# Performance work log

Hardware: AMD Instinct MI355X
Metric: run time of the kernel (lower is better)

The kernel has to match this reference:

```python
import jax, jax.numpy as jnp
import numpy as np

NUM_USERS = 100000
NUM_ITEMS = 50000
N_NODES = NUM_USERS + NUM_ITEMS
EMBED_DIM = 64
N_EDGES = 2400000
NUM_LAYERS = 3
DROPOUT_P = 0.2


def setup_inputs() -> dict:
    key = jax.random.key(0)
    k1, k2, k3, k4, k5 = jax.random.split(key, 5)
    # xavier_uniform bound = sqrt(6/(fan_in+fan_out))
    bu = np.sqrt(6.0 / (NUM_USERS + EMBED_DIM)).astype(np.float32)
    bi = np.sqrt(6.0 / (NUM_ITEMS + EMBED_DIM)).astype(np.float32)
    user_emb = jax.random.uniform(k1, (NUM_USERS, EMBED_DIM), jnp.float32, -bu, bu)
    item_emb = jax.random.uniform(k2, (NUM_ITEMS, EMBED_DIM), jnp.float32, -bi, bi)
    adj_rows = jax.random.randint(k3, (N_EDGES,), 0, N_NODES, dtype=jnp.int32)
    adj_cols = jax.random.randint(k4, (N_EDGES,), 0, N_NODES, dtype=jnp.int32)
    # normalized adjacency values (positive, small) mimicking D^-1/2 A D^-1/2
    adj_vals = jax.random.uniform(k5, (N_EDGES,), jnp.float32, 0.0, 0.25)
    return {"user_emb": user_emb, "item_emb": item_emb,
            "adj_rows": adj_rows, "adj_cols": adj_cols, "adj_vals": adj_vals}


def _spmm(rows, cols, vals, x):
    # y[r] += vals[e] * x[cols[e]] for each edge e with rows[e]==r
    gathered = x[cols] * vals[:, None]          # [E, D]
    return jax.ops.segment_sum(gathered, rows, num_segments=N_NODES)


def reference(user_emb, item_emb, adj_rows, adj_cols, adj_vals):
    x = jnp.concatenate([user_emb, item_emb], axis=0)          # [N, D]
    # dropout (training=True), fixed key for determinism
    keep = jax.random.bernoulli(jax.random.key(42), 1.0 - DROPOUT_P, x.shape)
    x = jnp.where(keep, x / (1.0 - DROPOUT_P), 0.0)
    acc = x  # running sum over layer embeddings (== mean * (L+1))
    for _ in range(NUM_LAYERS):
        x = _spmm(adj_rows, adj_cols, adj_vals, x)
        acc = acc + x
    final = acc / jnp.float32(NUM_LAYERS + 1)
    return final[:NUM_USERS], final[NUM_USERS:]
```

## Files before the change

kernel.cpp:

```cpp
#include <hip/hip_runtime.h>


static constexpr int NU = 100000;
static constexpr int NI = 50000;
static constexpr int NN = NU + NI;
static constexpr int D  = 64;
static constexpr int E  = 2400000;
static constexpr int XN = NN * D;
static constexpr int XH = XN / 2;
static constexpr int NB = (NN + 1023) >> 10;
static constexpr int BPC = 24000;
static constexpr int BIN_T = 256;
static constexpr int BIN_U = 16;
static constexpr int BIN_CHUNK = BIN_T * BIN_U;

typedef _Float16 half_t;
typedef _Float16 half8 __attribute__((ext_vector_type(8)));

__device__ __forceinline__ unsigned rotl32(unsigned x, int r) {
    return (x << r) | (x >> (32 - r));
}

__device__ __forceinline__ void threefry2x32(unsigned k0, unsigned k1,
                                             unsigned x0, unsigned x1,
                                             unsigned& o0, unsigned& o1) {
    unsigned ks2 = k0 ^ k1 ^ 0x1BD11BDAu;
    x0 += k0; x1 += k1;
#define TF_R(r) { x0 += x1; x1 = rotl32(x1, r); x1 ^= x0; }
    TF_R(13) TF_R(15) TF_R(26) TF_R(6)   x0 += k1;  x1 += ks2 + 1u;
    TF_R(17) TF_R(29) TF_R(16) TF_R(24)  x0 += ks2; x1 += k0 + 2u;
    TF_R(13) TF_R(15) TF_R(26) TF_R(6)   x0 += k0;  x1 += k1 + 3u;
    TF_R(17) TF_R(29) TF_R(16) TF_R(24)  x0 += k1;  x1 += ks2 + 4u;
    TF_R(13) TF_R(15) TF_R(26) TF_R(6)   x0 += ks2; x1 += k0 + 5u;
#undef TF_R
    o0 = x0; o1 = x1;
}

__device__ __forceinline__ float dropout_val(const float* __restrict__ ue,
                                             const float* __restrict__ ie,
                                             int i, unsigned bits) {
    float src = (i < NU * D) ? ue[i] : ie[i - NU * D];
    float u = __uint_as_float((bits >> 9) | 0x3f800000u) - 1.0f;
    return (u < 0.8f) ? (src / 0.8f) : 0.0f;
}

__global__ void k_dropout_init(const float* __restrict__ ue,
                               const float* __restrict__ ie,
                               half_t* __restrict__ x0h) {
    int j = blockIdx.x * blockDim.x + threadIdx.x;
    if (j >= XH) return;
    unsigned o0, o1, b0, b1;
    threefry2x32(0u, 42u, 0u, (unsigned)j, o0, o1);        b0 = o0 ^ o1;
    threefry2x32(0u, 42u, 0u, (unsigned)(j + XH), o0, o1); b1 = o0 ^ o1;
    x0h[j]      = (half_t)dropout_val(ue, ie, j, b0);
    x0h[j + XH] = (half_t)dropout_val(ue, ie, j + XH, b1);
}

__global__ void __launch_bounds__(BIN_T) k_bin(const int* __restrict__ rows,
                                               const int* __restrict__ cols,
                                               const float* __restrict__ vals,
                                               int2* __restrict__ stg,
                                               int* __restrict__ pcnt) {
    __shared__ int lcnt[NB];
    __shared__ int gbase[NB];
    int tid = threadIdx.x;
    for (int i = tid; i < NB; i += BIN_T) lcnt[i] = 0;
    __syncthreads();
    int base = blockIdx.x * BIN_CHUNK;
    int lp[BIN_U];
    int2 rec[BIN_U];
    #pragma unroll
    for (int u = 0; u < BIN_U; ++u) {
        int idx = base + u * BIN_T + tid;
        if (idx < E) {
            int row = rows[idx];
            int col = cols[idx];
            float v = vals[idx];
            unsigned q = min(__float2int_rn(v * 65536.f), 16383);
            int b = row >> 10;
            int loff = atomicAdd(&lcnt[b], 1);
            lp[u] = (b << 13) | loff;
            rec[u] = make_int2((int)((q << 18) | (unsigned)col), row);
        } else {
            lp[u] = -1;
        }
    }
    __syncthreads();
    for (int i = tid; i < NB; i += BIN_T)
        gbase[i] = atomicAdd(&pcnt[i * 16], lcnt[i]);
    __syncthreads();
    #pragma unroll
    for (int u = 0; u < BIN_U; ++u) {
        if (lp[u] >= 0) {
            int b = lp[u] >> 13;
            int pos = gbase[b] + (lp[u] & 8191);
            if (pos < BPC) stg[(size_t)b * BPC + pos] = rec[u];
        }
    }
}

__global__ void k_bscan(const int* __restrict__ pcnt, int* __restrict__ bbase,
                        int* __restrict__ rp) {
    int lane = threadIdx.x;
    int carry = 0;
    for (int base = 0; base < NB; base += 64) {
        int i = base + lane;
        int v = (i < NB) ? pcnt[i * 16] : 0;
        int x = v;
        #pragma unroll
        for (int d = 1; d < 64; d <<= 1) {
            int y = __shfl_up(x, d);
            if (lane >= d) x += y;
        }
        if (i < NB) bbase[i] = carry + x - v;
        carry += __shfl(x, 63);
    }
    if (lane == 0) rp[NN] = E;
}

__global__ void __launch_bounds__(1024) k_bsort(const int2* __restrict__ stg,
                                                const int* __restrict__ pcnt,
                                                const int* __restrict__ bbase,
                                                int* __restrict__ rp,
                                                unsigned* __restrict__ ev) {
    __shared__ int cnt[1024];
    __shared__ int wsum[16];
    int b = blockIdx.x;
    int t = threadIdx.x;
    cnt[t] = 0;
    __syncthreads();
    int tot = min(pcnt[b * 16], BPC);
    int bb = bbase[b];
    const int2* s = stg + (size_t)b * BPC;
    for (int i = t; i < tot; i += 1024)
        atomicAdd(&cnt[s[i].y & 1023], 1);
    __syncthreads();
    int v = cnt[t];
    int lane = t & 63, w = t >> 6;
    int x = v;
    #pragma unroll
    for (int d = 1; d < 64; d <<= 1) {
        int y = __shfl_up(x, d);
        if (lane >= d) x += y;
    }
    if (lane == 63) wsum[w] = x;
    __syncthreads();
    if (w == 0 && lane < 16) {
        int sv = wsum[lane];
        #pragma unroll
        for (int d = 1; d < 16; d <<= 1) {
            int y = __shfl_up(sv, d);
            if (lane >= d) sv += y;
        }
        wsum[lane] = sv;
    }
    __syncthreads();
    int excl = ((w > 0) ? wsum[w - 1] : 0) + x - v;
    int row = (b << 10) + t;
    if (row < NN) rp[row] = bb + excl;
    __syncthreads();
    cnt[t] = bb + excl;
    __syncthreads();
    for (int i = t; i < tot; i += 1024) {
        int2 r = s[i];
        int pos = atomicAdd(&cnt[r.y & 1023], 1);
        ev[pos] = (unsigned)r.x;
    }
}

template <int MODE>
__global__ void __launch_bounds__(256) k_spmm(const int* __restrict__ rp,
                                              const unsigned* __restrict__ ev,
                                              const half_t* __restrict__ xh,
                                              half_t* __restrict__ yh,
                                              const half_t* __restrict__ x0h,
                                              const half_t* __restrict__ y1h,
                                              float* __restrict__ out) {
    int wid  = threadIdx.x >> 6;
    int lane = threadIdx.x & 63;
    int g    = lane >> 3;
    int l    = lane & 7;
    int row  = blockIdx.x * 32 + wid * 8 + g;
    if (row >= NN) return;
    const float inv = 1.0f / 65536.0f;
    int s0  = rp[row];
    int cnt = rp[row + 1] - s0;
    float acc[8] = {0.f, 0.f, 0.f, 0.f, 0.f, 0.f, 0.f, 0.f};
    int gl = g << 3;
    for (int base = 0; base < cnt; base += 8) {
        int idx = base + l;
        int pc = (idx < cnt) ? (int)ev[s0 + idx] : 0;
        #pragma unroll
        for (int j = 0; j < 8; j += 2) {
            int p0 = __shfl(pc, gl | j);
            int p1 = __shfl(pc, gl | (j + 1));
            int   c0 = p0 & 0x3FFFF;
            float v0 = (float)((unsigned)p0 >> 18) * inv;
            int   c1 = p1 & 0x3FFFF;
            float v1 = (float)((unsigned)p1 >> 18) * inv;
            const half8 xa = *(const half8*)(xh + c0 * 64 + l * 8);
            const half8 xb = *(const half8*)(xh + c1 * 64 + l * 8);
            #pragma unroll
            for (int k = 0; k < 8; ++k) acc[k] = fmaf(v0, (float)xa[k], acc[k]);
            #pragma unroll
            for (int k = 0; k < 8; ++k) acc[k] = fmaf(v1, (float)xb[k], acc[k]);
        }
    }
    int o = row * 64 + l * 8;
    if (MODE == 0) {
        half8 st;
        #pragma unroll
        for (int k = 0; k < 8; ++k) st[k] = (half_t)acc[k];
        *(half8*)(yh + o) = st;
    } else {
        const half8 a0 = *(const half8*)(x0h + o);
        const half8 a1 = *(const half8*)(y1h + o);
        const half8 a2 = *(const half8*)(xh + o);
        float r[8];
        #pragma unroll
        for (int k = 0; k < 8; ++k)
            r[k] = ((float)a0[k] + (float)a1[k] + (float)a2[k] + acc[k]) * 0.25f;
        *(float4*)(out + o)     = make_float4(r[0], r[1], r[2], r[3]);
        *(float4*)(out + o + 4) = make_float4(r[4], r[5], r[6], r[7]);
    }
}

extern "C" void kernel_launch(void* const* d_in, const int* in_sizes, int n_in,
                              void* d_out, int out_size, void* d_ws, size_t ws_size,
                              hipStream_t stream) {
    const float* ue   = (const float*)d_in[0];
    const float* ie   = (const float*)d_in[1];
    const int*   rows = (const int*)d_in[2];
    const int*   cols = (const int*)d_in[3];
    const float* vals = (const float*)d_in[4];
    float* out = (float*)d_out;

    half_t*   X0h   = (half_t*)d_ws;
    half_t*   Y1h   = X0h + XN;
    half_t*   Y2h   = Y1h + XN;
    int2*     stg   = (int2*)Y1h;
    unsigned* ev    = (unsigned*)(Y2h + XN);
    int*      rp    = (int*)(ev + E);
    int*      pcnt  = rp + NN + 4;
    int*      bbase = pcnt + NB * 16;

    (void)hipMemsetAsync(pcnt, 0, (NB * 16 + NB) * sizeof(int), stream);
    k_dropout_init<<<(XH + 255) / 256, 256, 0, stream>>>(ue, ie, X0h);
    k_bin<<<(E + BIN_CHUNK - 1) / BIN_CHUNK, BIN_T, 0, stream>>>(rows, cols, vals, stg, pcnt);
    k_bscan<<<1, 64, 0, stream>>>(pcnt, bbase, rp);
    k_bsort<<<NB, 1024, 0, stream>>>(stg, pcnt, bbase, rp, ev);

    int sgrid = (NN + 31) / 32;
    k_spmm<0><<<sgrid, 256, 0, stream>>>(rp, ev, X0h, Y1h, nullptr, nullptr, nullptr);
    k_spmm<0><<<sgrid, 256, 0, stream>>>(rp, ev, Y1h, Y2h, nullptr, nullptr, nullptr);
    k_spmm<1><<<sgrid, 256, 0, stream>>>(rp, ev, Y2h, nullptr, X0h, Y1h, out);
}
```

Baseline: 318.6 us.

## Merge dropout into binning kernel, fold bucket scan into sort, batch SpMM gathers

Fuses the dropout-init kernel into the binning kernel as extra blocks and removes the single-block bucket scan by having each sort block compute its own prefix over bucket counts. This cuts two kernel launches and their serialization gaps. The SpMM inner loop now prefetches the next edge chunk and issues all eight row gathers before accumulating, to expose more memory-level parallelism. The cost is more registers in SpMM and a redundant O(NB) prefix sum per sort block.

```diff
diff --git a/kernel.cpp b/kernel.cpp
--- a/kernel.cpp
+++ b/kernel.cpp
@@ -13,6 +13,8 @@
 static constexpr int BIN_T = 256;
 static constexpr int BIN_U = 16;
 static constexpr int BIN_CHUNK = BIN_T * BIN_U;
+static constexpr int BGRID = (E + BIN_CHUNK - 1) / BIN_CHUNK;
+static constexpr int DGRID = (XH + 255) / 256;
 
 typedef _Float16 half_t;
 typedef _Float16 half8 __attribute__((ext_vector_type(8)));
@@ -44,26 +46,27 @@
     return (u < 0.8f) ? (src / 0.8f) : 0.0f;
 }
 
-__global__ void k_dropout_init(const float* __restrict__ ue,
-                               const float* __restrict__ ie,
-                               half_t* __restrict__ x0h) {
-    int j = blockIdx.x * blockDim.x + threadIdx.x;
-    if (j >= XH) return;
-    unsigned o0, o1, b0, b1;
-    threefry2x32(0u, 42u, 0u, (unsigned)j, o0, o1);        b0 = o0 ^ o1;
-    threefry2x32(0u, 42u, 0u, (unsigned)(j + XH), o0, o1); b1 = o0 ^ o1;
-    x0h[j]      = (half_t)dropout_val(ue, ie, j, b0);
-    x0h[j + XH] = (half_t)dropout_val(ue, ie, j + XH, b1);
-}
-
-__global__ void __launch_bounds__(BIN_T) k_bin(const int* __restrict__ rows,
+__global__ void __launch_bounds__(BIN_T) k_pre(const int* __restrict__ rows,
                                                const int* __restrict__ cols,
                                                const float* __restrict__ vals,
                                                int2* __restrict__ stg,
-                                               int* __restrict__ pcnt) {
+                                               int* __restrict__ pcnt,
+                                               const float* __restrict__ ue,
+                                               const float* __restrict__ ie,
+                                               half_t* __restrict__ x0h) {
     __shared__ int lcnt[NB];
     __shared__ int gbase[NB];
     int tid = threadIdx.x;
+    if (blockIdx.x >= BGRID) {
+        int j = (blockIdx.x - BGRID) * BIN_T + tid;
+        if (j >= XH) return;
+        unsigned o0, o1, b0, b1;
+        threefry2x32(0u, 42u, 0u, (unsigned)j, o0, o1);        b0 = o0 ^ o1;
+        threefry2x32(0u, 42u, 0u, (unsigned)(j + XH), o0, o1); b1 = o0 ^ o1;
+        x0h[j]      = (half_t)dropout_val(ue, ie, j, b0);
+        x0h[j + XH] = (half_t)dropout_val(ue, ie, j + XH, b1);
+        return;
+    }
     for (int i = tid; i < NB; i += BIN_T) lcnt[i] = 0;
     __syncthreads();
     int base = blockIdx.x * BIN_CHUNK;
@@ -99,38 +102,27 @@
     }
 }
 
-__global__ void k_bscan(const int* __restrict__ pcnt, int* __restrict__ bbase,
-                        int* __restrict__ rp) {
-    int lane = threadIdx.x;
-    int carry = 0;
-    for (int base = 0; base < NB; base += 64) {
-        int i = base + lane;
-        int v = (i < NB) ? pcnt[i * 16] : 0;
-        int x = v;
-        #pragma unroll
-        for (int d = 1; d < 64; d <<= 1) {
-            int y = __shfl_up(x, d);
-            if (lane >= d) x += y;
-        }
-        if (i < NB) bbase[i] = carry + x - v;
-        carry += __shfl(x, 63);
-    }
-    if (lane == 0) rp[NN] = E;
-}
-
 __global__ void __launch_bounds__(1024) k_bsort(const int2* __restrict__ stg,
                                                 const int* __restrict__ pcnt,
-                                                const int* __restrict__ bbase,
                                                 int* __restrict__ rp,
                                                 unsigned* __restrict__ ev) {
     __shared__ int cnt[1024];
     __shared__ int wsum[16];
+    __shared__ int sbb;
     int b = blockIdx.x;
     int t = threadIdx.x;
     cnt[t] = 0;
+    if (t < 64) {
+        int a = 0;
+        for (int i = t; i < b; i += 64) a += pcnt[i * 16];
+        #pragma unroll
+        for (int d = 1; d < 64; d <<= 1) a += __shfl_xor(a, d);
+        if (t == 0) sbb = a;
+    }
+    if (b == 0 && t == 0) rp[NN] = E;
     __syncthreads();
     int tot = min(pcnt[b * 16], BPC);
-    int bb = bbase[b];
+    int bb = sbb;
     const int2* s = stg + (size_t)b * BPC;
     for (int i = t; i < tot; i += 1024)
         atomicAdd(&cnt[s[i].y & 1023], 1);
@@ -187,24 +179,25 @@
     int cnt = rp[row + 1] - s0;
     float acc[8] = {0.f, 0.f, 0.f, 0.f, 0.f, 0.f, 0.f, 0.f};
     int gl = g << 3;
+    int pc = (l < cnt) ? (int)ev[s0 + l] : 0;
     for (int base = 0; base < cnt; base += 8) {
-        int idx = base + l;
-        int pc = (idx < cnt) ? (int)ev[s0 + idx] : 0;
-        #pragma unroll
-        for (int j = 0; j < 8; j += 2) {
-            int p0 = __shfl(pc, gl | j);
-            int p1 = __shfl(pc, gl | (j + 1));
-            int   c0 = p0 & 0x3FFFF;
-            float v0 = (float)((unsigned)p0 >> 18) * inv;
-            int   c1 = p1 & 0x3FFFF;
-            float v1 = (float)((unsigned)p1 >> 18) * inv;
-            const half8 xa = *(const half8*)(xh + c0 * 64 + l * 8);
-            const half8 xb = *(const half8*)(xh + c1 * 64 + l * 8);
+        int nidx = base + 8 + l;
+        int pcn = (nidx < cnt) ? (int)ev[s0 + nidx] : 0;
+        int pj[8];
+        #pragma unroll
+        for (int j = 0; j < 8; ++j) pj[j] = __shfl(pc, gl | j);
+        half8 xv[8];
+        #pragma unroll
+        for (int j = 0; j < 8; ++j)
+            xv[j] = *(const half8*)(xh + (pj[j] & 0x3FFFF) * 64 + l * 8);
+        #pragma unroll
+        for (int j = 0; j < 8; ++j) {
+            float vj = (float)((unsigned)pj[j] >> 18) * inv;
             #pragma unroll
-            for (int k = 0; k < 8; ++k) acc[k] = fmaf(v0, (float)xa[k], acc[k]);
-            #pragma unroll
-            for (int k = 0; k < 8; ++k) acc[k] = fmaf(v1, (float)xb[k], acc[k]);
-        }
+            for (int k = 0; k < 8; ++k)
+                acc[k] = fmaf(vj, (float)xv[j][k], acc[k]);
+        }
+        pc = pcn;
     }
     int o = row * 64 + l * 8;
     if (MODE == 0) {
@@ -242,13 +235,11 @@
     unsigned* ev    = (unsigned*)(Y2h + XN);
     int*      rp    = (int*)(ev + E);
     int*      pcnt  = rp + NN + 4;
-    int*      bbase = pcnt + NB * 16;
-
-    (void)hipMemsetAsync(pcnt, 0, (NB * 16 + NB) * sizeof(int), stream);
-    k_dropout_init<<<(XH + 255) / 256, 256, 0, stream>>>(ue, ie, X0h);
-    k_bin<<<(E + BIN_CHUNK - 1) / BIN_CHUNK, BIN_T, 0, stream>>>(rows, cols, vals, stg, pcnt);
-    k_bscan<<<1, 64, 0, stream>>>(pcnt, bbase, rp);
-    k_bsort<<<NB, 1024, 0, stream>>>(stg, pcnt, bbase, rp, ev);
+
+    (void)hipMemsetAsync(pcnt, 0, NB * 16 * sizeof(int), stream);
+    k_pre<<<BGRID + DGRID, BIN_T, 0, stream>>>(rows, cols, vals, stg, pcnt,
+                                               ue, ie, X0h);
+    k_bsort<<<NB, 1024, 0, stream>>>(stg, pcnt, rp, ev);
 
     int sgrid = (NN + 31) / 32;
     k_spmm<0><<<sgrid, 256, 0, stream>>>(rp, ev, X0h, Y1h, nullptr, nullptr, nullptr);
```

New measurement: 301.2 us. 5.5% less time.
